# Kernel tuning notes

Measured on AMD Instinct MI355X. Metric: run time of the kernel, lower is better.

## Reference

```python
import jax, jax.numpy as jnp
import numpy as np

B, N, D = 2, 2048, 1024
H = 16
DH = D // H
SCALE = 1.0 / np.sqrt(D).astype(np.float32)  # faithful: module uses 1/sqrt(d_out), not head_dim


def setup_inputs() -> dict:
    key = jax.random.key(0)
    ks = jax.random.split(key, 5)
    s = 0.02
    return {
        "x": jax.random.normal(ks[0], (B, N, D), dtype=jnp.float32),
        "Wq": jax.random.normal(ks[1], (D, D), dtype=jnp.float32) * s,
        "Wk": jax.random.normal(ks[2], (D, D), dtype=jnp.float32) * s,
        "Wv": jax.random.normal(ks[3], (D, D), dtype=jnp.float32) * s,
        "Wo": jax.random.normal(ks[4], (D, D), dtype=jnp.float32) * s,
        "bo": jnp.zeros((D,), dtype=jnp.float32),
    }


def reference(x, Wq, Wk, Wv, Wo, bo):
    b, n, _ = x.shape
    # qkv projections (no bias), split heads: [b, H, n, DH]
    q = (x @ Wq).reshape(b, n, H, DH).transpose(0, 2, 1, 3)
    k = (x @ Wk).reshape(b, n, H, DH).transpose(0, 2, 1, 3)
    v = (x @ Wv).reshape(b, n, H, DH).transpose(0, 2, 1, 3)
    # full N x N scores (the module materializes this)
    scores = jnp.einsum("bhqd,bhkd->bhqk", q, k)
    causal = jnp.triu(jnp.ones((n, n), dtype=bool), k=1)  # True above diagonal -> masked
    scores = jnp.where(causal[None, None], -jnp.inf, scores)
    # faithful order: mask first, then scale, then softmax (-inf * scale stays -inf)
    attn = jax.nn.softmax(scores * SCALE, axis=-1)
    ctx = jnp.einsum("bhqk,bhkd->bhqd", attn, v)
    ctx = ctx.transpose(0, 2, 1, 3).reshape(b, n, D)
    return ctx @ Wo + bo
```

## Files before the change

### kernel.cpp

```cpp
#include <hip/hip_runtime.h>
#include <stdint.h>

#define H 16
#define DH 64
#define BATCH 2
#define NSEQ 2048
#define DMODEL 1024
#define QSZ (BATCH*H*NSEQ*DH)
#define ATT_CS 0.04508422017f

typedef __attribute__((ext_vector_type(8))) short short8;
typedef __attribute__((ext_vector_type(4))) short shortx4;
typedef __attribute__((ext_vector_type(4))) float floatx4;

__device__ __forceinline__ short f2bf(float f) {
  union { float f; unsigned u; } c; c.f = f;
  unsigned u = c.u;
  unsigned r = (u + 0x7FFFu + ((u >> 16) & 1u)) >> 16;
  return (short)r;
}

__device__ __forceinline__ unsigned pk2bf(float a, float b) {
  union { float f; unsigned u; } ca, cb; ca.f = a; cb.f = b;
  return __builtin_amdgcn_perm(cb.u + 0x8000u, ca.u + 0x8000u, 0x07060302u);
}

__device__ __forceinline__ void gld_lds16(const short* g, short* l) {
  __builtin_amdgcn_global_load_lds((const __attribute__((address_space(1))) unsigned int*)g,
                                   (__attribute__((address_space(3))) unsigned int*)l,
                                   16, 0, 0);
}

__global__ __launch_bounds__(256) void prep_kernel(const float* __restrict__ x,
                                                   const float* __restrict__ Wq,
                                                   const float* __restrict__ Wk,
                                                   const float* __restrict__ Wv,
                                                   const float* __restrict__ Wo,
                                                   short* __restrict__ xb,
                                                   short* __restrict__ wqkvt,
                                                   short* __restrict__ wot) {
  __shared__ short tile[32][33];
  int bid = blockIdx.x;
  if (bid < 4096) {
    int i = bid * 256 + threadIdx.x;
    float4 v = ((const float4*)x)[i];
    short4 o;
    o.x = f2bf(v.x); o.y = f2bf(v.y); o.z = f2bf(v.z); o.w = f2bf(v.w);
    ((short4*)xb)[i] = o;
  } else {
    int t = bid - 4096;
    int widx = t >> 10, rem = t & 1023;
    int bx = rem & 31, by = rem >> 5;
    const float* W = (widx == 0) ? Wq : (widx == 1) ? Wk : (widx == 2) ? Wv : Wo;
    short* dst = (widx < 3) ? (wqkvt + (size_t)widx * 1048576) : wot;
    int k0 = bx * 32, n0 = by * 32;
    int tx = threadIdx.x & 31, ty = threadIdx.x >> 5;
#pragma unroll
    for (int i = 0; i < 4; i++) {
      int k = k0 + ty + i * 8;
      tile[tx][ty + i * 8] = f2bf(W[(size_t)k * DMODEL + n0 + tx]);
    }
    __syncthreads();
#pragma unroll
    for (int i = 0; i < 4; i++) {
      int n = n0 + ty + i * 8;
      dst[(size_t)n * DMODEL + k0 + tx] = tile[ty + i * 8][tx];
    }
  }
}

template <int MODE, int NT>
__global__ __launch_bounds__(256) void gemm_bt(const short* __restrict__ A,
                                               const short* __restrict__ Bt,
                                               short* __restrict__ outb,
                                               float* __restrict__ outf,
                                               const float* __restrict__ bias,
                                               int K, int nbn) {
  constexpr int JF = NT / 32;
  __shared__ __align__(16) short As[3][4096];
  __shared__ __align__(16) short Bs[3][NT * 32];
  int tid = threadIdx.x;
  int lane = tid & 63;
  int w = tid >> 6;
  int wm = w >> 1, wn = w & 1;
  int m16 = lane & 15, quad = lane >> 4;
  int hrow = m16 >> 1;
  int pb8 = (((((m16 & 1) << 2) | quad)) ^ hrow) << 3;
  int cpx = nbn >> 3;
  int xcd = blockIdx.x & 7, local = blockIdx.x >> 3;
  int bn = xcd * cpx + local % cpx;
  int bm = local / cpx;

  floatx4 acc[4][JF];
#pragma unroll
  for (int i = 0; i < 4; i++)
#pragma unroll
    for (int j = 0; j < JF; j++) acc[i][j] = (floatx4){0.f, 0.f, 0.f, 0.f};

  const short* Ablk = A + (size_t)bm * 128 * K;
  const short* Bblk = Bt + (size_t)bn * NT * K;

  auto stage = [&](int k0, int b) {
#pragma unroll
    for (int t = 0; t < 2; t++) {
      int e = w * 1024 + t * 512 + lane * 8;
      int l = ((e >> 3) & 7) ^ ((e >> 6) & 7);
      int row = ((e >> 6) << 1) | (l >> 2);
      int col = (l & 3) << 3;
      gld_lds16(Ablk + (size_t)row * K + k0 + col, &As[b][w * 1024 + t * 512]);
    }
    if constexpr (NT == 128) {
#pragma unroll
      for (int t = 0; t < 2; t++) {
        int e = w * 1024 + t * 512 + lane * 8;
        int l = ((e >> 3) & 7) ^ ((e >> 6) & 7);
        int row = ((e >> 6) << 1) | (l >> 2);
        int col = (l & 3) << 3;
        gld_lds16(Bblk + (size_t)row * K + k0 + col, &Bs[b][w * 1024 + t * 512]);
      }
    } else {
      int e = w * 512 + lane * 8;
      int l = ((e >> 3) & 7) ^ ((e >> 6) & 7);
      int row = ((e >> 6) << 1) | (l >> 2);
      int col = (l & 3) << 3;
      gld_lds16(Bblk + (size_t)row * K + k0 + col, &Bs[b][w * 512]);
    }
  };

  int nk = K >> 5;
  stage(0, 0);
  asm volatile("" ::: "memory");
  if (nk > 1) stage(32, 1);
  for (int kc = 0; kc < nk; kc++) {
    int b = kc % 3;
    if (kc + 1 < nk) {
      if constexpr (NT == 128) asm volatile("s_waitcnt vmcnt(4)\n\ts_barrier" ::: "memory");
      else                     asm volatile("s_waitcnt vmcnt(3)\n\ts_barrier" ::: "memory");
    } else {
      asm volatile("s_waitcnt vmcnt(0)\n\ts_barrier" ::: "memory");
    }
    short8 af[4], bfr[JF];
#pragma unroll
    for (int i = 0; i < 4; i++)
      af[i] = *(const short8*)&As[b][(wm * 32 + i * 8 + hrow) * 64 + pb8];
#pragma unroll
    for (int j = 0; j < JF; j++)
      bfr[j] = *(const short8*)&Bs[b][(wn * (NT / 4) + j * 8 + hrow) * 64 + pb8];
    if (kc + 2 < nk) stage((kc + 2) * 32, (kc + 2) % 3);
#pragma unroll
    for (int i = 0; i < 4; i++)
#pragma unroll
      for (int j = 0; j < JF; j++)
        acc[i][j] = __builtin_amdgcn_mfma_f32_16x16x32_bf16(af[i], bfr[j], acc[i][j], 0, 0, 0);
  }

  if constexpr (MODE == 0) {
    int which0 = (bn * NT) >> 10;
    if (which0 == 2) {
#pragma unroll
      for (int i = 0; i < 4; i++) {
        int mrow_base = bm * 128 + wm * 64 + i * 16 + quad * 4;
        int b = mrow_base >> 11, ns0 = mrow_base & 2047;
#pragma unroll
        for (int j = 0; j < JF; j++) {
          int ncol = bn * NT + wn * (NT / 2) + j * 16 + m16;
          int c = ncol & 1023;
          int h = c >> 6, dh = c & 63;
          shortx4 pk;
#pragma unroll
          for (int r = 0; r < 4; r++) pk[r] = f2bf(acc[i][j][r]);
          *(shortx4*)&outb[2 * (size_t)QSZ + (((size_t)(b * H + h) * DH + dh) * NSEQ) + ns0] = pk;
        }
      }
    } else {
      __syncthreads();
      float sc = (which0 == 0) ? ATT_CS : 1.0f;
      float* tp = ((float*)&As[0][0]) + w * 1024;
#pragma unroll
      for (int i = 0; i < 4; i++) {
        int mrow = bm * 128 + wm * 64 + i * 16 + m16;
        int b = mrow >> 11, ns = mrow & 2047;
#pragma unroll
        for (int j = 0; j < JF; j++) {
          int cbase = (bn * NT + wn * (NT / 2) + j * 16) & 1023;
          int h = cbase >> 6, dhb = cbase & 63;
          *(floatx4*)&tp[m16 * 20 + quad * 4] = acc[i][j];
          shortx4 pk;
#pragma unroll
          for (int cc = 0; cc < 4; cc++)
            pk[cc] = f2bf(tp[(quad * 4 + cc) * 20 + m16] * sc);
          *(shortx4*)&outb[(size_t)which0 * QSZ +
                           ((size_t)(b * H + h) * NSEQ + ns) * DH + dhb + quad * 4] = pk;
        }
      }
    }
  } else {
#pragma unroll
    for (int i = 0; i < 4; i++) {
      int mrow_base = bm * 128 + wm * 64 + i * 16 + quad * 4;
#pragma unroll
      for (int j = 0; j < JF; j++) {
        int ncol = bn * NT + wn * (NT / 2) + j * 16 + m16;
#pragma unroll
        for (int r = 0; r < 4; r++)
          outf[(size_t)(mrow_base + r) * DMODEL + ncol] = acc[i][j][r] + bias[ncol];
      }
    }
  }
}

__global__ __launch_bounds__(256) void attn_kernel(const short* __restrict__ Qw,
                                                   const short* __restrict__ Kw,
                                                   const short* __restrict__ VtG,
                                                   short* __restrict__ ctx) {
  __shared__ __align__(16) short Ks[2][4096];
  __shared__ __align__(16) short Vt[2][4096];
  __shared__ __align__(16) short Ps[2][4][16 * 72];
  int id = blockIdx.x;
  int bh = (id & 7) + ((id >> 7) << 3);
  int bx = (id >> 3) & 15;
  int tid = threadIdx.x, lane = tid & 63, w = tid >> 6;
  int m16 = lane & 15, quad = lane >> 4;
  int sw = m16 & 7;
  const size_t base = (size_t)bh * NSEQ * DH;
  const short* Kg0 = Kw + base;
  const short* Vg0 = VtG + base;
  short* PwA = &Ps[0][w][0];
  short* PwB = &Ps[1][w][0];

  int qbA = bx;
  int qbB = 31 - bx;
  int q0A = qbA * 64 + w * 16;
  int q0B = qbB * 64 + w * 16;

  short8 qfA[2], qfB[2];
#pragma unroll
  for (int kk = 0; kk < 2; kk++) {
    qfA[kk] = *(const short8*)(Qw + base + (size_t)(q0A + m16) * DH + kk * 32 + quad * 8);
    qfB[kk] = *(const short8*)(Qw + base + (size_t)(q0B + m16) * DH + kk * 32 + quad * 8);
  }

  float lA = 0.f, lB = 0.f;
  floatx4 oA[4], oB[4];
#pragma unroll
  for (int d = 0; d < 4; d++) { oA[d] = (floatx4){0.f,0.f,0.f,0.f}; oB[d] = (floatx4){0.f,0.f,0.f,0.f}; }

  short8 kf[4][2], vf[4][2];

  auto stage = [&](int kc, int sub) {
#pragma unroll
    for (int t = 0; t < 2; t++) {
      int e = w * 1024 + t * 512 + lane * 8;
      int r = e >> 6;
      int g = ((e >> 3) & 7) ^ (r & 7);
      gld_lds16(Kg0 + (size_t)(kc * 64 + r) * DH + g * 8, &Ks[sub][w * 1024 + t * 512]);
      gld_lds16(Vg0 + (size_t)r * NSEQ + kc * 64 + g * 8, &Vt[sub][w * 1024 + t * 512]);
    }
  };

  auto tile_qk = [&](bool diag, int kc, int q0, const short8* qf,
                     float& l, short* Pw) {
    floatx4 st[4];
#pragma unroll
    for (int nj = 0; nj < 4; nj++) {
      floatx4 s = (floatx4){0.f, 0.f, 0.f, 0.f};
      s = __builtin_amdgcn_mfma_f32_16x16x32_bf16(kf[nj][0], qf[0], s, 0, 0, 0);
      s = __builtin_amdgcn_mfma_f32_16x16x32_bf16(kf[nj][1], qf[1], s, 0, 0, 0);
      st[nj] = s;
    }
    int qrow = q0 + m16;
    float sum = 0.f;
#pragma unroll
    for (int nj = 0; nj < 4; nj++) {
      float p0 = __builtin_amdgcn_exp2f(st[nj][0]);
      float p1 = __builtin_amdgcn_exp2f(st[nj][1]);
      float p2 = __builtin_amdgcn_exp2f(st[nj][2]);
      float p3 = __builtin_amdgcn_exp2f(st[nj][3]);
      if (diag) {
        int key = kc * 64 + nj * 16 + quad * 4;
        p0 = (key     <= qrow) ? p0 : 0.f;
        p1 = (key + 1 <= qrow) ? p1 : 0.f;
        p2 = (key + 2 <= qrow) ? p2 : 0.f;
        p3 = (key + 3 <= qrow) ? p3 : 0.f;
      }
      sum += (p0 + p1) + (p2 + p3);
      uint2 pk;
      pk.x = pk2bf(p0, p1);
      pk.y = pk2bf(p2, p3);
      *(uint2*)&Pw[m16 * 72 + nj * 16 + quad * 4] = pk;
    }
    sum += __shfl_xor(sum, 16, 64);
    sum += __shfl_xor(sum, 32, 64);
    l += sum;
  };

  auto tile_pv = [&](floatx4* o, const short* Pw) {
    short8 pf[2];
    pf[0] = *(const short8*)&Pw[m16 * 72 + quad * 8];
    pf[1] = *(const short8*)&Pw[m16 * 72 + 32 + quad * 8];
#pragma unroll
    for (int d = 0; d < 4; d++) {
#pragma unroll
      for (int kj = 0; kj < 2; kj++)
        o[d] = __builtin_amdgcn_mfma_f32_16x16x32_bf16(vf[d][kj], pf[kj], o[d], 0, 0, 0);
    }
  };

  stage(0, 0);
  for (int kc = 0; kc <= qbB; kc++) {
    int b = kc & 1;
    __syncthreads();
#pragma unroll
    for (int nj = 0; nj < 4; nj++) {
      kf[nj][0] = *(const short8*)&Ks[b][(nj * 16 + m16) * 64 + ((quad ^ sw) * 8)];
      kf[nj][1] = *(const short8*)&Ks[b][(nj * 16 + m16) * 64 + (((4 + quad) ^ sw) * 8)];
    }
#pragma unroll
    for (int d = 0; d < 4; d++) {
      vf[d][0] = *(const short8*)&Vt[b][(d * 16 + m16) * 64 + ((quad ^ sw) * 8)];
      vf[d][1] = *(const short8*)&Vt[b][(d * 16 + m16) * 64 + (((4 + quad) ^ sw) * 8)];
    }
    if (kc + 1 <= qbB) stage(kc + 1, b ^ 1);
    if (kc <= qbA) {
      tile_qk(kc == qbA, kc, q0A, qfA, lA, PwA);
      tile_qk(false,     kc, q0B, qfB, lB, PwB);
      tile_pv(oA, PwA);
      tile_pv(oB, PwB);
    } else {
      tile_qk(kc == qbB, kc, q0B, qfB, lB, PwB);
      tile_pv(oB, PwB);
    }
  }

  int b = bh >> 4, h = bh & 15;
#pragma unroll
  for (int s = 0; s < 2; s++) {
    int q0 = s ? q0B : q0A;
    float inv = 1.f / (s ? lB : lA);
    floatx4* o = s ? oB : oA;
    size_t rowbase = ((size_t)(b * NSEQ + q0 + m16)) * DMODEL + h * DH;
#pragma unroll
    for (int d = 0; d < 4; d++) {
      shortx4 pk;
#pragma unroll
      for (int r = 0; r < 4; r++) pk[r] = f2bf(o[d][r] * inv);
      *(shortx4*)&ctx[rowbase + d * 16 + quad * 4] = pk;
    }
  }
}

extern "C" void kernel_launch(void* const* d_in, const int* in_sizes, int n_in,
                              void* d_out, int out_size, void* d_ws, size_t ws_size,
                              hipStream_t stream) {
  const float* x  = (const float*)d_in[0];
  const float* Wq = (const float*)d_in[1];
  const float* Wk = (const float*)d_in[2];
  const float* Wv = (const float*)d_in[3];
  const float* Wo = (const float*)d_in[4];
  const float* bo = (const float*)d_in[5];
  float* out = (float*)d_out;

  char* ws = (char*)d_ws;
  short* xb    = (short*)(ws);
  short* wqkvt = (short*)(ws + (8ull << 20));
  short* wot   = (short*)(ws + (14ull << 20));
  short* qkvws = (short*)(ws + (16ull << 20));
  short* ctx   = (short*)(ws + (40ull << 20));

  prep_kernel<<<8192, 256, 0, stream>>>(x, Wq, Wk, Wv, Wo, xb, wqkvt, wot);

  gemm_bt<0, 128><<<32 * 24, 256, 0, stream>>>(xb, wqkvt, qkvws, nullptr, nullptr, 1024, 24);

  short* qws = qkvws;
  short* kws = qkvws + QSZ;
  short* vtg = qkvws + 2 * QSZ;
  attn_kernel<<<512, 256, 0, stream>>>(qws, kws, vtg, ctx);

  gemm_bt<1, 64><<<32 * 16, 256, 0, stream>>>(ctx, wot, nullptr, out, bo, 1024, 16);
}
```

Measured before the change: 174.8 us.

## Split paired causal query blocks into one block per query tile

After: 185.8 us. 6.3% more time.

```diff
diff --git a/kernel.cpp b/kernel.cpp
--- a/kernel.cpp
+++ b/kernel.cpp
@@ -215,35 +215,29 @@
                                                    short* __restrict__ ctx) {
   __shared__ __align__(16) short Ks[2][4096];
   __shared__ __align__(16) short Vt[2][4096];
-  __shared__ __align__(16) short Ps[2][4][16 * 72];
+  __shared__ __align__(16) short Ps[4][16 * 72];
   int id = blockIdx.x;
-  int bh = (id & 7) + ((id >> 7) << 3);
-  int bx = (id >> 3) & 15;
+  int bh = (id & 7) + ((id >> 8) << 3);
+  int qb = (id >> 3) & 31;
   int tid = threadIdx.x, lane = tid & 63, w = tid >> 6;
   int m16 = lane & 15, quad = lane >> 4;
   int sw = m16 & 7;
   const size_t base = (size_t)bh * NSEQ * DH;
   const short* Kg0 = Kw + base;
   const short* Vg0 = VtG + base;
-  short* PwA = &Ps[0][w][0];
-  short* PwB = &Ps[1][w][0];
-
-  int qbA = bx;
-  int qbB = 31 - bx;
-  int q0A = qbA * 64 + w * 16;
-  int q0B = qbB * 64 + w * 16;
-
-  short8 qfA[2], qfB[2];
-#pragma unroll
-  for (int kk = 0; kk < 2; kk++) {
-    qfA[kk] = *(const short8*)(Qw + base + (size_t)(q0A + m16) * DH + kk * 32 + quad * 8);
-    qfB[kk] = *(const short8*)(Qw + base + (size_t)(q0B + m16) * DH + kk * 32 + quad * 8);
-  }
-
-  float lA = 0.f, lB = 0.f;
-  floatx4 oA[4], oB[4];
-#pragma unroll
-  for (int d = 0; d < 4; d++) { oA[d] = (floatx4){0.f,0.f,0.f,0.f}; oB[d] = (floatx4){0.f,0.f,0.f,0.f}; }
+  short* Pw = &Ps[w][0];
+
+  int q0 = qb * 64 + w * 16;
+
+  short8 qf[2];
+#pragma unroll
+  for (int kk = 0; kk < 2; kk++)
+    qf[kk] = *(const short8*)(Qw + base + (size_t)(q0 + m16) * DH + kk * 32 + quad * 8);
+
+  float l = 0.f;
+  floatx4 o[4];
+#pragma unroll
+  for (int d = 0; d < 4; d++) o[d] = (floatx4){0.f, 0.f, 0.f, 0.f};
 
   short8 kf[4][2], vf[4][2];
 
@@ -258,8 +252,7 @@
     }
   };
 
-  auto tile_qk = [&](bool diag, int kc, int q0, const short8* qf,
-                     float& l, short* Pw) {
+  auto tile_qk = [&](bool diag, int kc) {
     floatx4 st[4];
 #pragma unroll
     for (int nj = 0; nj < 4; nj++) {
@@ -294,7 +287,7 @@
     l += sum;
   };
 
-  auto tile_pv = [&](floatx4* o, const short* Pw) {
+  auto tile_pv = [&]() {
     short8 pf[2];
     pf[0] = *(const short8*)&Pw[m16 * 72 + quad * 8];
     pf[1] = *(const short8*)&Pw[m16 * 72 + 32 + quad * 8];
@@ -307,7 +300,7 @@
   };
 
   stage(0, 0);
-  for (int kc = 0; kc <= qbB; kc++) {
+  for (int kc = 0; kc <= qb; kc++) {
     int b = kc & 1;
     __syncthreads();
 #pragma unroll
@@ -320,32 +313,20 @@
       vf[d][0] = *(const short8*)&Vt[b][(d * 16 + m16) * 64 + ((quad ^ sw) * 8)];
       vf[d][1] = *(const short8*)&Vt[b][(d * 16 + m16) * 64 + (((4 + quad) ^ sw) * 8)];
     }
-    if (kc + 1 <= qbB) stage(kc + 1, b ^ 1);
-    if (kc <= qbA) {
-      tile_qk(kc == qbA, kc, q0A, qfA, lA, PwA);
-      tile_qk(false,     kc, q0B, qfB, lB, PwB);
-      tile_pv(oA, PwA);
-      tile_pv(oB, PwB);
-    } else {
-      tile_qk(kc == qbB, kc, q0B, qfB, lB, PwB);
-      tile_pv(oB, PwB);
-    }
-  }
-
-  int b = bh >> 4, h = bh & 15;
-#pragma unroll
-  for (int s = 0; s < 2; s++) {
-    int q0 = s ? q0B : q0A;
-    float inv = 1.f / (s ? lB : lA);
-    floatx4* o = s ? oB : oA;
-    size_t rowbase = ((size_t)(b * NSEQ + q0 + m16)) * DMODEL + h * DH;
-#pragma unroll
-    for (int d = 0; d < 4; d++) {
-      shortx4 pk;
-#pragma unroll
-      for (int r = 0; r < 4; r++) pk[r] = f2bf(o[d][r] * inv);
-      *(shortx4*)&ctx[rowbase + d * 16 + quad * 4] = pk;
-    }
+    if (kc + 1 <= qb) stage(kc + 1, b ^ 1);
+    tile_qk(kc == qb, kc);
+    tile_pv();
+  }
+
+  int bb = bh >> 4, h = bh & 15;
+  float inv = 1.f / l;
+  size_t rowbase = ((size_t)(bb * NSEQ + q0 + m16)) * DMODEL + h * DH;
+#pragma unroll
+  for (int d = 0; d < 4; d++) {
+    shortx4 pk;
+#pragma unroll
+    for (int r = 0; r < 4; r++) pk[r] = f2bf(o[d][r] * inv);
+    *(shortx4*)&ctx[rowbase + d * 16 + quad * 4] = pk;
   }
 }
 
@@ -374,7 +355,7 @@
   short* qws = qkvws;
   short* kws = qkvws + QSZ;
   short* vtg = qkvws + 2 * QSZ;
-  attn_kernel<<<512, 256, 0, stream>>>(qws, kws, vtg, ctx);
+  attn_kernel<<<1024, 256, 0, stream>>>(qws, kws, vtg, ctx);
 
   gemm_bt<1, 64><<<32 * 16, 256, 0, stream>>>(ctx, wot, nullptr, out, bo, 1024, 16);
 }
```
